# Performance work log

Measured on AMD Instinct MI355X. Metric: run time of the kernel, lower is better.

## Reference

```python
import jax, jax.numpy as jnp
import numpy as np

NUM_HEADS = 8
SCALE = 1.0
BN_EPS = 1e-5


def _mlp1d(x, W1, g1, b1, W2):
    # Conv1d(k=1, bias=False) -> BatchNorm1d (training-mode batch stats) -> ReLU -> Conv1d(k=1, bias=False)
    h = jnp.einsum('oi,bil->bol', W1, x)
    mu = h.mean(axis=(0, 2), keepdims=True)
    var = h.var(axis=(0, 2), keepdims=True)  # biased var, as torch BN training
    h = (h - mu) * jax.lax.rsqrt(var + BN_EPS)
    h = jax.nn.relu(h * g1[None, :, None] + b1[None, :, None])
    return jnp.einsum('oi,bil->bol', W2, h)


def setup_inputs() -> dict:
    key = jax.random.key(0)
    ks = jax.random.split(key, 8)
    b, c, hh, ww = 64, 2048, 14, 14
    hid, out = 4096, 256
    d = {'x': jax.random.normal(ks[0], (b, c, hh, ww), jnp.float32)}

    def w(k, o, i):
        return jax.random.normal(k, (o, i), jnp.float32) * np.float32(1.0 / np.sqrt(i))

    i = 1
    for pre in ('p', 'pp', 'po'):  # proj, proj_pixel, proj_obj
        d[pre + 'W1'] = w(ks[i], hid, c); i += 1
        d[pre + 'G1'] = jnp.ones((hid,), jnp.float32)
        d[pre + 'B1'] = jnp.zeros((hid,), jnp.float32)
        d[pre + 'W2'] = w(ks[i], out, hid); i += 1
    return d


def reference(x, pW1, pG1, pB1, pW2, ppW1, ppG1, ppB1, ppW2, poW1, poG1, poB1, poW2):
    b, c, h, w = x.shape
    xf = x.reshape(b, c, h * w)                      # flatten(2)
    x_pool = xf.mean(axis=2, keepdims=True)          # adaptive_avg_pool2d(x, 1)
    z_g = _mlp1d(x_pool, pW1, pG1, pB1, pW2)         # [b, 256, 1]
    z_feat = _mlp1d(xf, ppW1, ppG1, ppB1, ppW2)      # [b, 256, hw]
    # F.normalize(dim=1) with eps=1e-12, then /scale
    nrm = jnp.maximum(jnp.linalg.norm(z_feat, axis=1, keepdims=True), 1e-12)
    attn = (z_feat / nrm) / SCALE
    attn = attn.reshape(b, NUM_HEADS, -1, h * w)     # [b, nh, 256/nh, hw]
    attn = jax.nn.softmax(attn, axis=-1)
    x4 = xf.reshape(b, NUM_HEADS, c // NUM_HEADS, h * w)
    # torch.matmul(x, obj_attn.transpose(3, 2)) : [b,nh,c/nh,hw] @ [b,nh,hw,q]
    obj_val = jnp.einsum('bnkl,bnql->bnkq', x4, attn).reshape(b, c, -1)  # [b, c, 256/nh]
    obj_val = _mlp1d(obj_val, poW1, poG1, poB1, poW2)                    # [b, 256, 32]
    return z_g, obj_val
```

## Files before the change

### kernel.cpp

```cpp
#include <hip/hip_runtime.h>
#include <hip/hip_bf16.h>

using bf16 = __hip_bfloat16;
typedef __bf16 bf16x8v __attribute__((ext_vector_type(8)));
typedef float f32x4 __attribute__((ext_vector_type(4)));

#define BN_EPS 1e-5f

__device__ __forceinline__ void stval(float* p, float v) { *p = v; }
__device__ __forceinline__ void stval(bf16* p, float v)  { *p = __float2bfloat16(v); }

__device__ __forceinline__ void gload_lds16(const void* g, void* l) {
    __builtin_amdgcn_global_load_lds(
        (const __attribute__((address_space(1))) unsigned int*)g,
        (__attribute__((address_space(3))) unsigned int*)l,
        16, 0, 0);
}

__device__ __forceinline__ int xcd_swz(int orig, int nwg) {
    int q = nwg >> 3, r = nwg & 7;
    int xcd = orig & 7, idx = orig >> 3;
    return (xcd < r ? xcd * (q + 1) : r * (q + 1) + (xcd - r) * q) + idx;
}

template<typename TC>
__global__ __launch_bounds__(512, 2) void mfma_tn8(
    const bf16* __restrict__ A, const bf16* __restrict__ B, TC* __restrict__ C,
    int M, int N, int K, float* __restrict__ ps, float* __restrict__ pq)
{
    __shared__ char lds[131072];
    const int NT = K >> 6;
    const int tid = threadIdx.x;
    const int lane = tid & 63;
    const int wv = tid >> 6;
    const int wm = wv >> 2;
    const int wn = wv & 3;

    const int nbx = gridDim.x;
    int flat = blockIdx.y * nbx + blockIdx.x;
    const int cpx = (nbx * gridDim.y) >> 3;
    flat = (flat & 7) * cpx + (flat >> 3);
    const int mtile = flat / nbx;
    const long m0 = (long)mtile * 256;
    const long n0 = (long)(flat % nbx) * 256;

    const int trow = tid >> 3;
    const int ks = (((tid & 7) ^ ((tid >> 3) & 7)) << 3);
    const bf16* Arow0 = A + (m0 + trow) * (long)K + ks;
    const bf16* Brow0 = B + (n0 + trow) * (long)K + ks;
    char* ldsA = (char*)lds + tid * 16;
    char* ldsB = (char*)lds + 32768 + tid * 16;

    auto stage_a = [&](int bbuf, int kt) {
        const bf16* g = Arow0 + ((long)kt << 6);
        char* d = ldsA + (bbuf << 16);
        gload_lds16(g, d);
        gload_lds16(g + ((long)K << 6),  d + 8192);
        gload_lds16(g + ((long)K << 7),  d + 16384);
        gload_lds16(g + 192L * (long)K,  d + 24576);
    };
    auto stage_b = [&](int bbuf, int kt) {
        const bf16* g = Brow0 + ((long)kt << 6);
        char* d = ldsB + (bbuf << 16);
        gload_lds16(g, d);
        gload_lds16(g + ((long)K << 6),  d + 8192);
        gload_lds16(g + ((long)K << 7),  d + 16384);
        gload_lds16(g + 192L * (long)K,  d + 24576);
    };

    const int fr = lane & 15, fc = lane >> 4;
    const int ca0 = ((fc ^ (fr & 7)) << 4);
    const int ca1 = (((4 + fc) ^ (fr & 7)) << 4);

    f32x4 acc[8][4];
#pragma unroll
    for (int m = 0; m < 8; ++m)
#pragma unroll
        for (int n = 0; n < 4; ++n) acc[m][n] = (f32x4){0.f, 0.f, 0.f, 0.f};

    stage_a(0, 0); stage_b(0, 0); stage_a(1, 1); stage_b(1, 1);

    for (int T = 0; T < NT; ++T) {
        const int bb = T & 1;
        const char* Ard = (const char*)lds + (bb << 16) + (wm * 128 + fr) * 128;
        const char* Brd = (const char*)lds + (bb << 16) + 32768 + (wn * 64 + fr) * 128;

        if (T == 0)          { asm volatile("s_waitcnt vmcnt(8)" ::: "memory"); }
        else if (T < NT - 1) { asm volatile("s_waitcnt vmcnt(4)" ::: "memory"); }
        else                 { asm volatile("s_waitcnt vmcnt(0)" ::: "memory"); }
        __builtin_amdgcn_s_barrier();
        __builtin_amdgcn_sched_barrier(0);

        bf16x8v a0[8], a1[8];
#pragma unroll
        for (int m = 0; m < 8; ++m) {
            a0[m] = *(const bf16x8v*)(Ard + m * 2048 + ca0);
            a1[m] = *(const bf16x8v*)(Ard + m * 2048 + ca1);
        }
        bf16x8v b00 = *(const bf16x8v*)(Brd + ca0);
        bf16x8v b01 = *(const bf16x8v*)(Brd + ca1);
        bf16x8v b10 = *(const bf16x8v*)(Brd + 2048 + ca0);
        bf16x8v b11 = *(const bf16x8v*)(Brd + 2048 + ca1);

        if (T >= 1 && T + 1 < NT) stage_b(bb ^ 1, T + 1);

        __builtin_amdgcn_s_setprio(1);
#pragma unroll
        for (int m = 0; m < 8; ++m) {
            acc[m][0] = __builtin_amdgcn_mfma_f32_16x16x32_bf16(a0[m], b00, acc[m][0], 0, 0, 0);
            acc[m][0] = __builtin_amdgcn_mfma_f32_16x16x32_bf16(a1[m], b01, acc[m][0], 0, 0, 0);
            acc[m][1] = __builtin_amdgcn_mfma_f32_16x16x32_bf16(a0[m], b10, acc[m][1], 0, 0, 0);
            acc[m][1] = __builtin_amdgcn_mfma_f32_16x16x32_bf16(a1[m], b11, acc[m][1], 0, 0, 0);
        }
        __builtin_amdgcn_s_setprio(0);

        __builtin_amdgcn_s_barrier();
        __builtin_amdgcn_sched_barrier(0);

        bf16x8v b20 = *(const bf16x8v*)(Brd + 2 * 2048 + ca0);
        bf16x8v b21 = *(const bf16x8v*)(Brd + 2 * 2048 + ca1);
        bf16x8v b30 = *(const bf16x8v*)(Brd + 3 * 2048 + ca0);
        bf16x8v b31 = *(const bf16x8v*)(Brd + 3 * 2048 + ca1);

        if (T + 2 < NT) stage_a(bb, T + 2);

        __builtin_amdgcn_s_setprio(1);
#pragma unroll
        for (int m = 0; m < 8; ++m) {
            acc[m][2] = __builtin_amdgcn_mfma_f32_16x16x32_bf16(a0[m], b20, acc[m][2], 0, 0, 0);
            acc[m][2] = __builtin_amdgcn_mfma_f32_16x16x32_bf16(a1[m], b21, acc[m][2], 0, 0, 0);
            acc[m][3] = __builtin_amdgcn_mfma_f32_16x16x32_bf16(a0[m], b30, acc[m][3], 0, 0, 0);
            acc[m][3] = __builtin_amdgcn_mfma_f32_16x16x32_bf16(a1[m], b31, acc[m][3], 0, 0, 0);
        }
        __builtin_amdgcn_s_setprio(0);
    }

#pragma unroll
    for (int m = 0; m < 8; ++m) {
        long gr = m0 + wm * 128 + m * 16 + fc * 4;
#pragma unroll
        for (int n = 0; n < 4; ++n) {
            long gc = n0 + wn * 64 + n * 16 + fr;
            TC* cp = C + gr * N + gc;
#pragma unroll
            for (int r = 0; r < 4; ++r) stval(cp + (long)r * N, acc[m][n][r]);
        }
    }

    if (ps != nullptr) {
        __syncthreads();
        float* red = (float*)lds;
        float cs[4], cq[4];
#pragma unroll
        for (int n = 0; n < 4; ++n) {
            float s = 0.f, q = 0.f;
#pragma unroll
            for (int m = 0; m < 8; ++m)
#pragma unroll
                for (int r = 0; r < 4; ++r) {
                    float v = __bfloat162float(__float2bfloat16(acc[m][n][r]));
                    s += v; q += v * v;
                }
            s += __shfl_xor(s, 16, 64); s += __shfl_xor(s, 32, 64);
            q += __shfl_xor(q, 16, 64); q += __shfl_xor(q, 32, 64);
            cs[n] = s; cq[n] = q;
        }
        if (fc == 0) {
#pragma unroll
            for (int n = 0; n < 4; ++n) {
                red[wv * 64 + n * 16 + fr] = cs[n];
                red[512 + wv * 64 + n * 16 + fr] = cq[n];
            }
        }
        __syncthreads();
        if (tid < 256) {
            int c = tid, wnn = c >> 6, idx = c & 63;
            float s = red[wnn * 64 + idx] + red[(4 + wnn) * 64 + idx];
            float q = red[512 + wnn * 64 + idx] + red[512 + (4 + wnn) * 64 + idx];
            ps[(long)mtile * N + n0 + c] = s;
            pq[(long)mtile * N + n0 + c] = q;
        }
    }
}

template<typename TC>
__global__ __launch_bounds__(256) void mfma_tn(
    const bf16* __restrict__ A, const bf16* __restrict__ B, TC* __restrict__ C,
    int M, int N, int K, float* __restrict__ ps, float* __restrict__ pq)
{
    __shared__ alignas(16) unsigned short As[128 * 32];
    __shared__ alignas(16) unsigned short Bs[128 * 32];

    const int tid = threadIdx.x;
    const int l = tid & 63;
    const int nwg = gridDim.x * gridDim.y;
    int s = xcd_swz(blockIdx.y * gridDim.x + blockIdx.x, nwg);
    const int by = s / gridDim.x, bx = s % gridDim.x;
    const long m0 = (long)by * 128;
    const long n0 = (long)bx * 128;
    const int wr = (tid >> 7) & 1;
    const int wc = (tid >> 6) & 1;

    const int off0 = tid * 16;
    const int row0 = off0 >> 6;
    const int kp0  = (off0 >> 4) & 3;
    const bf16* Ag0 = A + (m0 + row0) * (long)K + kp0 * 8;
    const bf16* Ag1 = A + (m0 + row0 + 64) * (long)K + kp0 * 8;
    const bf16* Bg0 = B + (n0 + row0) * (long)K + kp0 * 8;
    const bf16* Bg1 = B + (n0 + row0 + 64) * (long)K + kp0 * 8;
    char* Asl0 = (char*)As + off0;
    char* Asl1 = (char*)As + off0 + 4096;
    char* Bsl0 = (char*)Bs + off0;
    char* Bsl1 = (char*)Bs + off0 + 4096;

    f32x4 acc[4][4];
#pragma unroll
    for (int m = 0; m < 4; ++m)
#pragma unroll
        for (int n = 0; n < 4; ++n) acc[m][n] = (f32x4){0.f, 0.f, 0.f, 0.f};

    const int fr = l & 15;
    const int fc = l >> 4;
    int aoff[4], boff[4];
#pragma unroll
    for (int m = 0; m < 4; ++m) aoff[m] = ((wr * 64 + m * 16 + fr) * 4 + fc) * 16;
#pragma unroll
    for (int n = 0; n < 4; ++n) boff[n] = ((wc * 64 + n * 16 + fr) * 4 + fc) * 16;

    for (int k0 = 0; k0 < K; k0 += 32) {
        gload_lds16(Ag0 + k0, Asl0);
        gload_lds16(Ag1 + k0, Asl1);
        gload_lds16(Bg0 + k0, Bsl0);
        gload_lds16(Bg1 + k0, Bsl1);
        __syncthreads();

        bf16x8v af[4], bfr[4];
#pragma unroll
        for (int m = 0; m < 4; ++m) af[m]  = *(const bf16x8v*)((const char*)As + aoff[m]);
#pragma unroll
        for (int n = 0; n < 4; ++n) bfr[n] = *(const bf16x8v*)((const char*)Bs + boff[n]);
#pragma unroll
        for (int m = 0; m < 4; ++m)
#pragma unroll
            for (int n = 0; n < 4; ++n)
                acc[m][n] = __builtin_amdgcn_mfma_f32_16x16x32_bf16(af[m], bfr[n], acc[m][n], 0, 0, 0);
        __syncthreads();
    }

#pragma unroll
    for (int m = 0; m < 4; ++m) {
        long gr = m0 + wr * 64 + m * 16 + fc * 4;
#pragma unroll
        for (int n = 0; n < 4; ++n) {
            long gc = n0 + wc * 64 + n * 16 + fr;
            TC* cp = C + gr * N + gc;
#pragma unroll
            for (int r = 0; r < 4; ++r) stval(cp + (long)r * N, acc[m][n][r]);
        }
    }

    if (ps != nullptr) {
        float* red = (float*)As;
        float cs[4], cq[4];
#pragma unroll
        for (int n = 0; n < 4; ++n) {
            float s2 = 0.f, q2 = 0.f;
#pragma unroll
            for (int m = 0; m < 4; ++m)
#pragma unroll
                for (int r = 0; r < 4; ++r) {
                    float v = __bfloat162float(__float2bfloat16(acc[m][n][r]));
                    s2 += v; q2 += v * v;
                }
            s2 += __shfl_xor(s2, 16, 64); s2 += __shfl_xor(s2, 32, 64);
            q2 += __shfl_xor(q2, 16, 64); q2 += __shfl_xor(q2, 32, 64);
            cs[n] = s2; cq[n] = q2;
        }
        if (fc == 0) {
#pragma unroll
            for (int n = 0; n < 4; ++n) {
                int c = wc * 64 + n * 16 + fr;
                red[wr * 128 + c] = cs[n];
                red[256 + wr * 128 + c] = cq[n];
            }
        }
        __syncthreads();
        if (tid < 128) {
            float sv = red[tid] + red[128 + tid];
            float qv = red[256 + tid] + red[384 + tid];
            ps[(long)by * N + n0 + tid] = sv;
            pq[(long)by * N + n0 + tid] = qv;
        }
    }
}

__global__ __launch_bounds__(256) void mfma_tn_skbn(
    const bf16* __restrict__ A, const bf16* __restrict__ B, float* __restrict__ Cp,
    int M, int N, int K, int KCH, const float* __restrict__ ta, const float* __restrict__ tc)
{
    __shared__ alignas(16) unsigned short As[128 * 32];
    __shared__ alignas(16) unsigned short Bs[128 * 32];

    const int tid = threadIdx.x;
    const int l = tid & 63;
    const int gxy = gridDim.x * gridDim.y;
    const int nwg = gxy * gridDim.z;
    int s = xcd_swz((blockIdx.z * gridDim.y + blockIdx.y) * gridDim.x + blockIdx.x, nwg);
    const int bz = s / gxy;
    const int rem = s % gxy;
    const int by = rem / gridDim.x, bx = rem % gridDim.x;
    const long m0 = (long)by * 128;
    const long n0 = (long)bx * 128;
    const int wr = (tid >> 7) & 1;
    const int wc = (tid >> 6) & 1;
    const int ksrt = bz * KCH;

    const int off0 = tid * 16;
    const int row0 = off0 >> 6;
    const int kp0  = (off0 >> 4) & 3;
    const bf16* Ag0 = A + (m0 + row0) * (long)K + kp0 * 8 + ksrt;
    const bf16* Ag1 = A + (m0 + row0 + 64) * (long)K + kp0 * 8 + ksrt;
    const bf16* Bg0 = B + (n0 + row0) * (long)K + kp0 * 8 + ksrt;
    const bf16* Bg1 = B + (n0 + row0 + 64) * (long)K + kp0 * 8 + ksrt;
    char* Asl0 = (char*)As + off0;
    char* Asl1 = (char*)As + off0 + 4096;
    char* Bsl0 = (char*)Bs + off0;
    char* Bsl1 = (char*)Bs + off0 + 4096;

    f32x4 acc[4][4];
#pragma unroll
    for (int m = 0; m < 4; ++m)
#pragma unroll
        for (int n = 0; n < 4; ++n) acc[m][n] = (f32x4){0.f, 0.f, 0.f, 0.f};

    const int fr = l & 15;
    const int fc = l >> 4;
    int aoff[4], boff[4];
#pragma unroll
    for (int m = 0; m < 4; ++m) aoff[m] = ((wr * 64 + m * 16 + fr) * 4 + fc) * 16;
#pragma unroll
    for (int n = 0; n < 4; ++n) boff[n] = ((wc * 64 + n * 16 + fr) * 4 + fc) * 16;

    for (int k0 = 0; k0 < KCH; k0 += 32) {
        gload_lds16(Bg0 + k0, Bsl0);
        gload_lds16(Bg1 + k0, Bsl1);

        union { bf16 h[8]; uint4 u; } r0, r1;
        r0.u = *(const uint4*)(Ag0 + k0);
        r1.u = *(const uint4*)(Ag1 + k0);
        const int kb = ksrt + k0 + kp0 * 8;
        float4 av0 = *(const float4*)(ta + kb);
        float4 av1 = *(const float4*)(ta + kb + 4);
        float4 cv0 = *(const float4*)(tc + kb);
        float4 cv1 = *(const float4*)(tc + kb + 4);
        float av[8] = {av0.x, av0.y, av0.z, av0.w, av1.x, av1.y, av1.z, av1.w};
        float cv[8] = {cv0.x, cv0.y, cv0.z, cv0.w, cv1.x, cv1.y, cv1.z, cv1.w};
#pragma unroll
        for (int j = 0; j < 8; ++j) {
            float v = fmaxf(fmaf(av[j], __bfloat162float(r0.h[j]), cv[j]), 0.f);
            r0.h[j] = __float2bfloat16(v);
            v = fmaxf(fmaf(av[j], __bfloat162float(r1.h[j]), cv[j]), 0.f);
            r1.h[j] = __float2bfloat16(v);
        }
        *(uint4*)Asl0 = r0.u;
        *(uint4*)Asl1 = r1.u;
        __syncthreads();

        bf16x8v af[4], bfr[4];
#pragma unroll
        for (int m = 0; m < 4; ++m) af[m]  = *(const bf16x8v*)((const char*)As + aoff[m]);
#pragma unroll
        for (int n = 0; n < 4; ++n) bfr[n] = *(const bf16x8v*)((const char*)Bs + boff[n]);
#pragma unroll
        for (int m = 0; m < 4; ++m)
#pragma unroll
            for (int n = 0; n < 4; ++n)
                acc[m][n] = __builtin_amdgcn_mfma_f32_16x16x32_bf16(af[m], bfr[n], acc[m][n], 0, 0, 0);
        __syncthreads();
    }

    float* Cb = Cp + (long)bz * M * N;
#pragma unroll
    for (int m = 0; m < 4; ++m) {
        long gr = m0 + wr * 64 + m * 16 + fc * 4;
#pragma unroll
        for (int n = 0; n < 4; ++n) {
            long gc = n0 + wc * 64 + n * 16 + fr;
            float* cp = Cb + gr * N + gc;
#pragma unroll
            for (int r = 0; r < 4; ++r) cp[(long)r * N] = acc[m][n][r];
        }
    }
}

__global__ __launch_bounds__(256) void objmm_k(
    const bf16* __restrict__ attnP, const bf16* __restrict__ xP, bf16* __restrict__ objinT)
{
    __shared__ alignas(16) unsigned short As[32 * 32];
    __shared__ alignas(16) unsigned short Bs[256 * 32];
    const int tid = threadIdx.x, lane = tid & 63, wv = tid >> 6;
    const int b = blockIdx.x >> 3, h = blockIdx.x & 7;
    const bf16* Ab = attnP + ((long)(b * 256 + h * 32)) * 224;
    const bf16* Bb = xP + ((long)(b * 2048 + h * 256)) * 224;
    const int fr = lane & 15, fc = lane >> 4;
    const int srow = tid >> 2, schk = tid & 3;

    f32x4 acc[2][4];
#pragma unroll
    for (int m = 0; m < 2; ++m)
#pragma unroll
        for (int n = 0; n < 4; ++n) acc[m][n] = (f32x4){0.f, 0.f, 0.f, 0.f};

    for (int k0 = 0; k0 < 224; k0 += 32) {
        if (wv < 2)
            gload_lds16(Ab + (long)srow * 224 + schk * 8 + k0, (char*)As + tid * 16);
#pragma unroll
        for (int j = 0; j < 4; ++j)
            gload_lds16(Bb + (long)(j * 64 + srow) * 224 + schk * 8 + k0,
                        (char*)Bs + j * 4096 + tid * 16);
        __syncthreads();

        bf16x8v af[2], bfr[4];
#pragma unroll
        for (int m = 0; m < 2; ++m)
            af[m] = *(const bf16x8v*)((const char*)As + (m * 16 + fr) * 64 + fc * 16);
#pragma unroll
        for (int n = 0; n < 4; ++n)
            bfr[n] = *(const bf16x8v*)((const char*)Bs + (wv * 64 + n * 16 + fr) * 64 + fc * 16);
#pragma unroll
        for (int m = 0; m < 2; ++m)
#pragma unroll
            for (int n = 0; n < 4; ++n)
                acc[m][n] = __builtin_amdgcn_mfma_f32_16x16x32_bf16(af[m], bfr[n], acc[m][n], 0, 0, 0);
        __syncthreads();
    }

#pragma unroll
    for (int m = 0; m < 2; ++m) {
        long gr = (long)b * 32 + m * 16 + fc * 4;
#pragma unroll
        for (int n = 0; n < 4; ++n) {
            long gc = (long)h * 256 + wv * 64 + n * 16 + fr;
            bf16* cp = objinT + gr * 2048 + gc;
#pragma unroll
            for (int r = 0; r < 4; ++r) cp[(long)r * 2048] = __float2bfloat16(acc[m][n][r]);
        }
    }
}

__global__ __launch_bounds__(256) void foldnorm_k(const float* __restrict__ p,
    float* __restrict__ z, float* __restrict__ invn)
{
    int j = blockIdx.x * 4 + (threadIdx.x >> 6);
    int lane = threadIdx.x & 63;
    long off = (long)j * 256 + lane * 4;
    float4 a = *(const float4*)(p + off);
    float4 b = *(const float4*)(p + 3211264L + off);
    float4 c = *(const float4*)(p + 2 * 3211264L + off);
    float4 d = *(const float4*)(p + 3 * 3211264L + off);
    float4 s;
    s.x = (a.x + b.x) + (c.x + d.x);
    s.y = (a.y + b.y) + (c.y + d.y);
    s.z = (a.z + b.z) + (c.z + d.z);
    s.w = (a.w + b.w) + (c.w + d.w);
    *(float4*)(z + off) = s;
    float q = s.x * s.x + s.y * s.y + s.z * s.z + s.w * s.w;
#pragma unroll
    for (int off2 = 32; off2; off2 >>= 1) q += __shfl_xor(q, off2, 64);
    if (lane == 0) invn[j] = 1.f / fmaxf(sqrtf(q), 1e-12f);
}

__global__ __launch_bounds__(256) void foldout_k(const float* __restrict__ p, float* __restrict__ out)
{
    int o = blockIdx.x * 256 + threadIdx.x;
    int b = o >> 13, rem = o & 8191, q = rem >> 5, tt = rem & 31;
    long base = ((long)(b * 32 + tt)) * 256 + q;
    float s = 0.f;
#pragma unroll
    for (int z = 0; z < 8; ++z) s += p[(long)z * 524288 + base];
    out[o] = s;
}

__global__ __launch_bounds__(256) void prep_k(
    const float* __restrict__ w1, const float* __restrict__ w2,
    const float* __restrict__ w3, const float* __restrict__ w4,
    bf16* __restrict__ o1, bf16* __restrict__ o2,
    bf16* __restrict__ o3, bf16* __restrict__ o4,
    const float* __restrict__ x, bf16* __restrict__ XT,
    bf16* __restrict__ xP, float* __restrict__ xpT)
{
    __shared__ unsigned short tile[196 * 66 + 4];
    __shared__ float pp[64];
    const int t = threadIdx.x;

    if (blockIdx.x < 9216) {
        const long L1 = 8388608, L2 = 1048576;
        long i = ((long)blockIdx.x * 256 + t) * 8;
        const float* src; bf16* dst; long e;
        if (i < L1)             { src = w1; dst = o1; e = i; }
        else if (i < L1 + L2)   { src = w2; dst = o2; e = i - L1; }
        else if (i < 2*L1 + L2) { src = w3; dst = o3; e = i - L1 - L2; }
        else                    { src = w4; dst = o4; e = i - 2*L1 - L2; }
        float4 v0 = *(const float4*)(src + e);
        float4 v1 = *(const float4*)(src + e + 4);
        union { bf16 h[8]; uint4 u; } r;
        r.h[0] = __float2bfloat16(v0.x); r.h[1] = __float2bfloat16(v0.y);
        r.h[2] = __float2bfloat16(v0.z); r.h[3] = __float2bfloat16(v0.w);
        r.h[4] = __float2bfloat16(v1.x); r.h[5] = __float2bfloat16(v1.y);
        r.h[6] = __float2bfloat16(v1.z); r.h[7] = __float2bfloat16(v1.w);
        *(uint4*)(dst + e) = r.u;
        return;
    }

    const int bid = blockIdx.x - 9216;
    const int b = bid >> 5, c0 = (bid & 31) * 64;
    const int wvi = t >> 6, lane = t & 63;

    for (int p = 0; p < 16; ++p) {
        int c = p * 4 + wvi;
        const float* row = x + ((long)b * 2048 + c0 + c) * 196;
        float v0 = row[lane];
        float v1 = row[lane + 64];
        float v2 = row[lane + 128];
        float v3 = (lane < 4) ? row[lane + 192] : 0.f;
        bf16 h0 = __float2bfloat16(v0);
        bf16 h1 = __float2bfloat16(v1);
        bf16 h2 = __float2bfloat16(v2);
        bf16 h3 = __float2bfloat16(v3);
        tile[lane * 66 + c]         = *(unsigned short*)&h0;
        tile[(lane + 64) * 66 + c]  = *(unsigned short*)&h1;
        tile[(lane + 128) * 66 + c] = *(unsigned short*)&h2;
        if (lane < 4) tile[(lane + 192) * 66 + c] = *(unsigned short*)&h3;
        float s = v0 + v1 + v2 + v3;
#pragma unroll
        for (int off = 32; off; off >>= 1) s += __shfl_xor(s, off, 64);
        if (lane == 0) pp[c] = s;
    }
    __syncthreads();
    if (t < 64) xpT[(c0 + t) * 64 + b] = pp[t] * (1.f / 196.f);

    for (int u = t; u < 196 * 8; u += 256) {
        int l = u >> 3, cc = u & 7;
        const unsigned short* sp = &tile[l * 66 + cc * 8];
        uint4 r;
        r.x = *(const unsigned int*)(sp);
        r.y = *(const unsigned int*)(sp + 2);
        r.z = *(const unsigned int*)(sp + 4);
        r.w = *(const unsigned int*)(sp + 6);
        *(uint4*)(&XT[((long)b * 196 + l) * 2048 + c0 + cc * 8]) = r;
    }

    for (int u = t; u < 64 * 28; u += 256) {
        int c = u / 28, ch = u % 28;
        int l0 = ch * 8;
        union { unsigned short h[8]; uint4 v; } r;
#pragma unroll
        for (int e = 0; e < 8; ++e) {
            int ll = l0 + e;
            r.h[e] = (ll < 196) ? tile[ll * 66 + c] : (unsigned short)0;
        }
        *(uint4*)(xP + ((long)b * 2048 + c0 + c) * 224 + l0) = r.v;
    }
}

__global__ __launch_bounds__(256) void colstat2_k(const float* __restrict__ ps, const float* __restrict__ pq,
    int P, float invN, const float* __restrict__ g, const float* __restrict__ be,
    float* __restrict__ ta, float* __restrict__ tc)
{
    int c = blockIdx.x * 256 + threadIdx.x;
    float s = 0.f, q = 0.f;
    for (int p = 0; p < P; ++p) { s += ps[(long)p * 4096 + c]; q += pq[(long)p * 4096 + c]; }
    float mu  = s * invN;
    float var = q * invN - mu * mu;
    float a   = g[c] * rsqrtf(var + BN_EPS);
    ta[c] = a;
    tc[c] = be[c] - mu * a;
}

__global__ __launch_bounds__(256) void softmax2_k(const float* __restrict__ z,
    const float* __restrict__ invn, bf16* __restrict__ attnP)
{
    int row  = blockIdx.x * 4 + (threadIdx.x >> 6);
    int lane = threadIdx.x & 63;
    int b = row >> 8, q = row & 255;
    float v[4];
    float mx = -INFINITY;
#pragma unroll
    for (int i = 0; i < 4; ++i) {
        int l = lane + 64 * i;
        if (l < 196) {
            int j = b * 196 + l;
            v[i] = z[(long)j * 256 + q] * invn[j];
        } else v[i] = -INFINITY;
        mx = fmaxf(mx, v[i]);
    }
#pragma unroll
    for (int off = 32; off; off >>= 1) mx = fmaxf(mx, __shfl_xor(mx, off, 64));
    float s = 0.f;
#pragma unroll
    for (int i = 0; i < 4; ++i) {
        v[i] = (lane + 64 * i < 196) ? __expf(v[i] - mx) : 0.f;
        s += v[i];
    }
#pragma unroll
    for (int off = 32; off; off >>= 1) s += __shfl_xor(s, off, 64);
    float is = 1.f / s;
    bf16* rp = attnP + (long)row * 224;
#pragma unroll
    for (int i = 0; i < 4; ++i) {
        int l = lane + 64 * i;
        if (l < 196) rp[l] = __float2bfloat16(v[i] * is);
        else if (l < 224) rp[l] = __float2bfloat16(0.f);
    }
}

template<bool TRANS>
__global__ __launch_bounds__(256) void gemmsk_k(
    const float* __restrict__ A, const float* __restrict__ B, float* __restrict__ Cp,
    int M, int N, int K, int lda, int ldbk, int KCH,
    const float* __restrict__ tra, const float* __restrict__ trc)
{
    constexpr int BM = 64, BN = 64, BK = 16;
    __shared__ float As[BK][BM + 4];
    __shared__ float Bs[BK][BN + 4];

    const int tid = threadIdx.x;
    const int m0 = blockIdx.y * BM;
    const int ks = blockIdx.z * KCH;
    const int ke = min(K, ks + KCH);

    const int tIdm = tid / 16;
    const int tIdn = tid % 16;
    const int aK  = tid % BK;
    const int aM0 = tid / BK;
    const int bN  = tid % BN;
    const int bK0 = tid / BN;

    float acc[4][4];
#pragma unroll
    for (int u = 0; u < 4; ++u)
#pragma unroll
        for (int v = 0; v < 4; ++v) acc[u][v] = 0.f;

    for (int k0 = ks; k0 < ke; k0 += BK) {
#pragma unroll
        for (int i = 0; i < 4; ++i) {
            int m = aM0 + 16 * i;
            int gk = k0 + aK, gm = m0 + m;
            float v = 0.f;
            if (gk < ke && gm < M) v = A[(long)gm * lda + gk];
            As[aK][m] = v;
        }
#pragma unroll
        for (int i = 0; i < 4; ++i) {
            int kk = bK0 + 4 * i;
            int gk = k0 + kk;
            float v = 0.f;
            if (gk < ke && bN < N) {
                v = B[(long)gk * ldbk + bN];
                if (TRANS) v = fmaxf(tra[gk] * v + trc[gk], 0.f);
            }
            Bs[kk][bN] = v;
        }
        __syncthreads();
#pragma unroll
        for (int kk = 0; kk < BK; ++kk) {
            float a[4], b[4];
#pragma unroll
            for (int u = 0; u < 4; ++u) a[u] = As[kk][tIdm * 4 + u];
#pragma unroll
            for (int v = 0; v < 4; ++v) b[v] = Bs[kk][tIdn * 4 + v];
#pragma unroll
            for (int u = 0; u < 4; ++u)
#pragma unroll
                for (int v = 0; v < 4; ++v)
                    acc[u][v] = fmaf(a[u], b[v], acc[u][v]);
        }
        __syncthreads();
    }

    float* Cb = Cp + (long)blockIdx.z * M * N;
#pragma unroll
    for (int u = 0; u < 4; ++u) {
        int gm = m0 + tIdm * 4 + u;
        if (gm >= M) continue;
#pragma unroll
        for (int v = 0; v < 4; ++v) {
            int gn = tIdn * 4 + v;
            if (gn < N) Cb[(long)gm * N + gn] = acc[u][v];
        }
    }
}

__global__ __launch_bounds__(256) void skbn_k(const float* __restrict__ Cp,
    const float* __restrict__ g, const float* __restrict__ be,
    float* __restrict__ h1, float* __restrict__ ta, float* __restrict__ tc)
{
    int o = blockIdx.x * 4 + (threadIdx.x >> 6);
    int b = threadIdx.x & 63;
    float s = 0.f;
#pragma unroll
    for (int p = 0; p < 16; ++p) s += Cp[(long)p * 262144 + o * 64 + b];
    h1[o * 64 + b] = s;
    float s1 = s, s2 = s * s;
#pragma unroll
    for (int off = 32; off; off >>= 1) {
        s1 += __shfl_down(s1, off, 64);
        s2 += __shfl_down(s2, off, 64);
    }
    if (b == 0) {
        float mu  = s1 * (1.f / 64.f);
        float var = s2 * (1.f / 64.f) - mu * mu;
        float a   = g[o] * rsqrtf(var + BN_EPS);
        ta[o] = a;
        tc[o] = be[o] - mu * a;
    }
}

__global__ __launch_bounds__(256) void skreduce_k(const float* __restrict__ Cp, int P, long MN,
    int Nn, int ldm, int ldn, float* __restrict__ out)
{
    long i = (long)blockIdx.x * 256 + threadIdx.x;
    if (i >= MN) return;
    float s = 0.f;
    for (int p = 0; p < P; ++p) s += Cp[(long)p * MN + i];
    int m = (int)(i / Nn), n = (int)(i % Nn);
    out[(long)m * ldm + (long)n * ldn] = s;
}

extern "C" void kernel_launch(void* const* d_in, const int* in_sizes, int n_in,
                              void* d_out, int out_size, void* d_ws, size_t ws_size,
                              hipStream_t stream)
{
    const float* x    = (const float*)d_in[0];
    const float* pW1  = (const float*)d_in[1];
    const float* pG1  = (const float*)d_in[2];
    const float* pB1  = (const float*)d_in[3];
    const float* pW2  = (const float*)d_in[4];
    const float* ppW1 = (const float*)d_in[5];
    const float* ppG1 = (const float*)d_in[6];
    const float* ppB1 = (const float*)d_in[7];
    const float* ppW2 = (const float*)d_in[8];
    const float* poW1 = (const float*)d_in[9];
    const float* poG1 = (const float*)d_in[10];
    const float* poB1 = (const float*)d_in[11];
    const float* poW2 = (const float*)d_in[12];
    float* out = (float*)d_out;
    (void)in_sizes; (void)n_in; (void)out_size; (void)ws_size;

    char* w = (char*)d_ws;
    auto alloc = [&](size_t bytes) -> char* {
        char* p = w; w += (bytes + 255) & ~(size_t)255; return p;
    };
    bf16* ppW1b = (bf16*)alloc((size_t)4096 * 2048 * 2);
    bf16* ppW2b = (bf16*)alloc((size_t)256 * 4096 * 2);
    bf16* poW1b = (bf16*)alloc((size_t)4096 * 2048 * 2);
    bf16* poW2b = (bf16*)alloc((size_t)256 * 4096 * 2);
    char* region1 = alloc((size_t)12544 * 2048 * 2);
    bf16*  XT     = (bf16*)region1;
    float* skpG2  = (float*)region1;
    bf16*  attnP  = (bf16*)region1;
    bf16*  objinT = (bf16*)(region1 + 12845056);
    bf16*  hobjT  = (bf16*)(region1 + 12845056 + 8388608);
    bf16* xP     = (bf16*)alloc((size_t)64 * 2048 * 224 * 2);
    bf16* hfeatT = (bf16*)alloc((size_t)12544 * 4096 * 2);
    float* zfeatT = (float*)alloc((size_t)12544 * 256 * 4);
    float* ps    = (float*)alloc((size_t)49 * 4096 * 4);
    float* pq    = (float*)alloc((size_t)49 * 4096 * 4);
    float* invn  = (float*)alloc((size_t)12544 * 4);
    float* a2    = (float*)alloc(4096 * 4);
    float* c2    = (float*)alloc(4096 * 4);
    float* a3    = (float*)alloc(4096 * 4);
    float* c3    = (float*)alloc(4096 * 4);
    float* xpT   = (float*)alloc((size_t)2048 * 64 * 4);
    float* h1    = (float*)alloc((size_t)4096 * 64 * 4);
    float* a1    = (float*)alloc(4096 * 4);
    float* c1    = (float*)alloc(4096 * 4);
    float* skp1  = (float*)alloc((size_t)16 * 4096 * 64 * 4);
    float* skp2  = (float*)alloc((size_t)32 * 256 * 64 * 4);
    float* skp5  = (float*)alloc((size_t)8 * 2048 * 256 * 4);

    prep_k<<<9216 + 2048, 256, 0, stream>>>(ppW1, ppW2, poW1, poW2,
                                            ppW1b, ppW2b, poW1b, poW2b,
                                            x, XT, xP, xpT);

    gemmsk_k<false><<<dim3(1, 64, 16), 256, 0, stream>>>(
        pW1, xpT, skp1, 4096, 64, 2048, 2048, 64, 128, nullptr, nullptr);
    skbn_k<<<1024, 256, 0, stream>>>(skp1, pG1, pB1, h1, a1, c1);
    gemmsk_k<true><<<dim3(1, 4, 32), 256, 0, stream>>>(
        pW2, h1, skp2, 256, 64, 4096, 4096, 64, 128, a1, c1);
    skreduce_k<<<64, 256, 0, stream>>>(skp2, 32, (long)256 * 64, 64, 1, 256, out);

    mfma_tn8<bf16><<<dim3(16, 49), 512, 0, stream>>>(XT, ppW1b, hfeatT, 12544, 4096, 2048, ps, pq);
    colstat2_k<<<16, 256, 0, stream>>>(ps, pq, 49, 1.f / 12544.f, ppG1, ppB1, a2, c2);

    mfma_tn_skbn<<<dim3(2, 98, 4), 256, 0, stream>>>(
        hfeatT, ppW2b, skpG2, 12544, 256, 4096, 1024, a2, c2);
    foldnorm_k<<<3136, 256, 0, stream>>>(skpG2, zfeatT, invn);

    softmax2_k<<<4096, 256, 0, stream>>>(zfeatT, invn, attnP);

    objmm_k<<<512, 256, 0, stream>>>(attnP, xP, objinT);

    mfma_tn<bf16><<<dim3(32, 16), 256, 0, stream>>>(objinT, poW1b, hobjT, 2048, 4096, 2048, ps, pq);
    colstat2_k<<<16, 256, 0, stream>>>(ps, pq, 16, 1.f / 2048.f, poG1, poB1, a3, c3);

    mfma_tn_skbn<<<dim3(2, 16, 8), 256, 0, stream>>>(
        hobjT, poW2b, skp5, 2048, 256, 4096, 512, a3, c3);
    foldout_k<<<2048, 256, 0, stream>>>(skp5, out + 16384);
}
```

Baseline: 609.7 us.

## Shrink big GEMM tile to 256x128 with K=32 steps and fold skreduce into foldnorm

Replaces the 256x256, K=64 tile of the main feature GEMM with a 256x128 tile using K=32 steps. It uses less LDS (48KB) and targets 4 blocks per CU, trading per-block reuse for higher occupancy and a larger grid. The LDS XOR swizzle is removed, so LDS bank conflicts may increase. The split-K reduction for z_g is also moved into extra blocks of foldnorm_k, removing one kernel launch.

Result: no change. 619.8 us (+1.7%).

```diff
diff --git a/kernel.cpp b/kernel.cpp
--- a/kernel.cpp
+++ b/kernel.cpp
@@ -23,18 +23,20 @@
     return (xcd < r ? xcd * (q + 1) : r * (q + 1) + (xcd - r) * q) + idx;
 }
 
+#define MFMA_BF16 __builtin_amdgcn_mfma_f32_16x16x32_bf16
+
 template<typename TC>
-__global__ __launch_bounds__(512, 2) void mfma_tn8(
+__global__ __launch_bounds__(512, 4) void mfma_tn8c(
     const bf16* __restrict__ A, const bf16* __restrict__ B, TC* __restrict__ C,
     int M, int N, int K, float* __restrict__ ps, float* __restrict__ pq)
 {
-    __shared__ char lds[131072];
-    const int NT = K >> 6;
+    __shared__ alignas(16) char lds[49152];
+    const int NT = K >> 5;
     const int tid = threadIdx.x;
     const int lane = tid & 63;
     const int wv = tid >> 6;
-    const int wm = wv >> 2;
-    const int wn = wv & 3;
+    const int wm = wv >> 1;
+    const int wn = wv & 1;
 
     const int nbx = gridDim.x;
     int flat = blockIdx.y * nbx + blockIdx.x;
@@ -42,39 +44,30 @@
     flat = (flat & 7) * cpx + (flat >> 3);
     const int mtile = flat / nbx;
     const long m0 = (long)mtile * 256;
-    const long n0 = (long)(flat % nbx) * 256;
-
-    const int trow = tid >> 3;
-    const int ks = (((tid & 7) ^ ((tid >> 3) & 7)) << 3);
-    const bf16* Arow0 = A + (m0 + trow) * (long)K + ks;
-    const bf16* Brow0 = B + (n0 + trow) * (long)K + ks;
-    char* ldsA = (char*)lds + tid * 16;
-    char* ldsB = (char*)lds + 32768 + tid * 16;
+    const long n0 = (long)(flat % nbx) * 128;
+
+    const int trow = tid >> 2;
+    const int tk   = (tid & 3) * 8;
+    const bf16* Ar = A + (m0 + trow) * (long)K + tk;
+    const bf16* Br = B + (n0 + trow) * (long)K + tk;
+    char* ldsAt = (char*)lds + tid * 16;
+    char* ldsBt = (char*)lds + 32768 + tid * 16;
 
     auto stage_a = [&](int bbuf, int kt) {
-        const bf16* g = Arow0 + ((long)kt << 6);
-        char* d = ldsA + (bbuf << 16);
+        const bf16* g = Ar + (kt << 5);
+        char* d = ldsAt + bbuf * 16384;
         gload_lds16(g, d);
-        gload_lds16(g + ((long)K << 6),  d + 8192);
-        gload_lds16(g + ((long)K << 7),  d + 16384);
-        gload_lds16(g + 192L * (long)K,  d + 24576);
+        gload_lds16(g + ((long)K << 7), d + 8192);
     };
     auto stage_b = [&](int bbuf, int kt) {
-        const bf16* g = Brow0 + ((long)kt << 6);
-        char* d = ldsB + (bbuf << 16);
-        gload_lds16(g, d);
-        gload_lds16(g + ((long)K << 6),  d + 8192);
-        gload_lds16(g + ((long)K << 7),  d + 16384);
-        gload_lds16(g + 192L * (long)K,  d + 24576);
+        gload_lds16(Br + (kt << 5), ldsBt + bbuf * 8192);
     };
 
     const int fr = lane & 15, fc = lane >> 4;
-    const int ca0 = ((fc ^ (fr & 7)) << 4);
-    const int ca1 = (((4 + fc) ^ (fr & 7)) << 4);
-
-    f32x4 acc[8][4];
-#pragma unroll
-    for (int m = 0; m < 8; ++m)
+
+    f32x4 acc[4][4];
+#pragma unroll
+    for (int m = 0; m < 4; ++m)
 #pragma unroll
         for (int n = 0; n < 4; ++n) acc[m][n] = (f32x4){0.f, 0.f, 0.f, 0.f};
 
@@ -82,62 +75,51 @@
 
     for (int T = 0; T < NT; ++T) {
         const int bb = T & 1;
-        const char* Ard = (const char*)lds + (bb << 16) + (wm * 128 + fr) * 128;
-        const char* Brd = (const char*)lds + (bb << 16) + 32768 + (wn * 64 + fr) * 128;
-
-        if (T == 0)          { asm volatile("s_waitcnt vmcnt(8)" ::: "memory"); }
-        else if (T < NT - 1) { asm volatile("s_waitcnt vmcnt(4)" ::: "memory"); }
+        const char* Ard = (const char*)lds + bb * 16384 + (wm * 64 + fr) * 64 + fc * 16;
+        const char* Brd = (const char*)lds + 32768 + bb * 8192 + (wn * 64 + fr) * 64 + fc * 16;
+
+        if (T == 0)          { asm volatile("s_waitcnt vmcnt(3)" ::: "memory"); }
+        else if (T < NT - 1) { asm volatile("s_waitcnt vmcnt(2)" ::: "memory"); }
         else                 { asm volatile("s_waitcnt vmcnt(0)" ::: "memory"); }
         __builtin_amdgcn_s_barrier();
         __builtin_amdgcn_sched_barrier(0);
 
-        bf16x8v a0[8], a1[8];
-#pragma unroll
-        for (int m = 0; m < 8; ++m) {
-            a0[m] = *(const bf16x8v*)(Ard + m * 2048 + ca0);
-            a1[m] = *(const bf16x8v*)(Ard + m * 2048 + ca1);
-        }
-        bf16x8v b00 = *(const bf16x8v*)(Brd + ca0);
-        bf16x8v b01 = *(const bf16x8v*)(Brd + ca1);
-        bf16x8v b10 = *(const bf16x8v*)(Brd + 2048 + ca0);
-        bf16x8v b11 = *(const bf16x8v*)(Brd + 2048 + ca1);
+        bf16x8v a[4];
+#pragma unroll
+        for (int m = 0; m < 4; ++m) a[m] = *(const bf16x8v*)(Ard + m * 1024);
+        bf16x8v b0 = *(const bf16x8v*)(Brd);
+        bf16x8v b1 = *(const bf16x8v*)(Brd + 1024);
 
         if (T >= 1 && T + 1 < NT) stage_b(bb ^ 1, T + 1);
 
         __builtin_amdgcn_s_setprio(1);
 #pragma unroll
-        for (int m = 0; m < 8; ++m) {
-            acc[m][0] = __builtin_amdgcn_mfma_f32_16x16x32_bf16(a0[m], b00, acc[m][0], 0, 0, 0);
-            acc[m][0] = __builtin_amdgcn_mfma_f32_16x16x32_bf16(a1[m], b01, acc[m][0], 0, 0, 0);
-            acc[m][1] = __builtin_amdgcn_mfma_f32_16x16x32_bf16(a0[m], b10, acc[m][1], 0, 0, 0);
-            acc[m][1] = __builtin_amdgcn_mfma_f32_16x16x32_bf16(a1[m], b11, acc[m][1], 0, 0, 0);
+        for (int m = 0; m < 4; ++m) {
+            acc[m][0] = MFMA_BF16(a[m], b0, acc[m][0], 0, 0, 0);
+            acc[m][1] = MFMA_BF16(a[m], b1, acc[m][1], 0, 0, 0);
         }
         __builtin_amdgcn_s_setprio(0);
 
         __builtin_amdgcn_s_barrier();
         __builtin_amdgcn_sched_barrier(0);
 
-        bf16x8v b20 = *(const bf16x8v*)(Brd + 2 * 2048 + ca0);
-        bf16x8v b21 = *(const bf16x8v*)(Brd + 2 * 2048 + ca1);
-        bf16x8v b30 = *(const bf16x8v*)(Brd + 3 * 2048 + ca0);
-        bf16x8v b31 = *(const bf16x8v*)(Brd + 3 * 2048 + ca1);
+        bf16x8v b2 = *(const bf16x8v*)(Brd + 2048);
+        bf16x8v b3 = *(const bf16x8v*)(Brd + 3072);
 
         if (T + 2 < NT) stage_a(bb, T + 2);
 
         __builtin_amdgcn_s_setprio(1);
 #pragma unroll
-        for (int m = 0; m < 8; ++m) {
-            acc[m][2] = __builtin_amdgcn_mfma_f32_16x16x32_bf16(a0[m], b20, acc[m][2], 0, 0, 0);
-            acc[m][2] = __builtin_amdgcn_mfma_f32_16x16x32_bf16(a1[m], b21, acc[m][2], 0, 0, 0);
-            acc[m][3] = __builtin_amdgcn_mfma_f32_16x16x32_bf16(a0[m], b30, acc[m][3], 0, 0, 0);
-            acc[m][3] = __builtin_amdgcn_mfma_f32_16x16x32_bf16(a1[m], b31, acc[m][3], 0, 0, 0);
+        for (int m = 0; m < 4; ++m) {
+            acc[m][2] = MFMA_BF16(a[m], b2, acc[m][2], 0, 0, 0);
+            acc[m][3] = MFMA_BF16(a[m], b3, acc[m][3], 0, 0, 0);
         }
         __builtin_amdgcn_s_setprio(0);
     }
 
 #pragma unroll
-    for (int m = 0; m < 8; ++m) {
-        long gr = m0 + wm * 128 + m * 16 + fc * 4;
+    for (int m = 0; m < 4; ++m) {
+        long gr = m0 + wm * 64 + m * 16 + fc * 4;
 #pragma unroll
         for (int n = 0; n < 4; ++n) {
             long gc = n0 + wn * 64 + n * 16 + fr;
@@ -155,7 +137,7 @@
         for (int n = 0; n < 4; ++n) {
             float s = 0.f, q = 0.f;
 #pragma unroll
-            for (int m = 0; m < 8; ++m)
+            for (int m = 0; m < 4; ++m)
 #pragma unroll
                 for (int r = 0; r < 4; ++r) {
                     float v = __bfloat162float(__float2bfloat16(acc[m][n][r]));
@@ -168,17 +150,17 @@
         if (fc == 0) {
 #pragma unroll
             for (int n = 0; n < 4; ++n) {
-                red[wv * 64 + n * 16 + fr] = cs[n];
-                red[512 + wv * 64 + n * 16 + fr] = cq[n];
+                int c = wn * 64 + n * 16 + fr;
+                red[wm * 128 + c] = cs[n];
+                red[512 + wm * 128 + c] = cq[n];
             }
         }
         __syncthreads();
-        if (tid < 256) {
-            int c = tid, wnn = c >> 6, idx = c & 63;
-            float s = red[wnn * 64 + idx] + red[(4 + wnn) * 64 + idx];
-            float q = red[512 + wnn * 64 + idx] + red[512 + (4 + wnn) * 64 + idx];
-            ps[(long)mtile * N + n0 + c] = s;
-            pq[(long)mtile * N + n0 + c] = q;
+        if (tid < 128) {
+            float s = red[tid] + red[128 + tid] + red[256 + tid] + red[384 + tid];
+            float q = red[512 + tid] + red[640 + tid] + red[768 + tid] + red[896 + tid];
+            ps[(long)mtile * N + n0 + tid] = s;
+            pq[(long)mtile * N + n0 + tid] = q;
         }
     }
 }
@@ -243,7 +225,7 @@
         for (int m = 0; m < 4; ++m)
 #pragma unroll
             for (int n = 0; n < 4; ++n)
-                acc[m][n] = __builtin_amdgcn_mfma_f32_16x16x32_bf16(af[m], bfr[n], acc[m][n], 0, 0, 0);
+                acc[m][n] = MFMA_BF16(af[m], bfr[n], acc[m][n], 0, 0, 0);
         __syncthreads();
     }
 
@@ -375,7 +357,7 @@
         for (int m = 0; m < 4; ++m)
 #pragma unroll
             for (int n = 0; n < 4; ++n)
-                acc[m][n] = __builtin_amdgcn_mfma_f32_16x16x32_bf16(af[m], bfr[n], acc[m][n], 0, 0, 0);
+                acc[m][n] = MFMA_BF16(af[m], bfr[n], acc[m][n], 0, 0, 0);
         __syncthreads();
     }
 
@@ -431,7 +413,7 @@
         for (int m = 0; m < 2; ++m)
 #pragma unroll
             for (int n = 0; n < 4; ++n)
-                acc[m][n] = __builtin_amdgcn_mfma_f32_16x16x32_bf16(af[m], bfr[n], acc[m][n], 0, 0, 0);
+                acc[m][n] = MFMA_BF16(af[m], bfr[n], acc[m][n], 0, 0, 0);
         __syncthreads();
     }
 
@@ -449,8 +431,17 @@
 }
 
 __global__ __launch_bounds__(256) void foldnorm_k(const float* __restrict__ p,
-    float* __restrict__ z, float* __restrict__ invn)
-{
+    float* __restrict__ z, float* __restrict__ invn,
+    const float* __restrict__ skp2, float* __restrict__ out)
+{
+    if (blockIdx.x >= 3136) {
+        int i = (blockIdx.x - 3136) * 256 + threadIdx.x;
+        float s = 0.f;
+        for (int pz = 0; pz < 32; ++pz) s += skp2[(long)pz * 16384 + i];
+        int m = i >> 6, n = i & 63;
+        out[m + n * 256] = s;
+        return;
+    }
     int j = blockIdx.x * 4 + (threadIdx.x >> 6);
     int lane = threadIdx.x & 63;
     long off = (long)j * 256 + lane * 4;
@@ -715,17 +706,6 @@
         ta[o] = a;
         tc[o] = be[o] - mu * a;
     }
-}
-
-__global__ __launch_bounds__(256) void skreduce_k(const float* __restrict__ Cp, int P, long MN,
-    int Nn, int ldm, int ldn, float* __restrict__ out)
-{
-    long i = (long)blockIdx.x * 256 + threadIdx.x;
-    if (i >= MN) return;
-    float s = 0.f;
-    for (int p = 0; p < P; ++p) s += Cp[(long)p * MN + i];
-    int m = (int)(i / Nn), n = (int)(i % Nn);
-    out[(long)m * ldm + (long)n * ldn] = s;
 }
 
 extern "C" void kernel_launch(void* const* d_in, const int* in_sizes, int n_in,
@@ -789,14 +769,13 @@
     skbn_k<<<1024, 256, 0, stream>>>(skp1, pG1, pB1, h1, a1, c1);
     gemmsk_k<true><<<dim3(1, 4, 32), 256, 0, stream>>>(
         pW2, h1, skp2, 256, 64, 4096, 4096, 64, 128, a1, c1);
-    skreduce_k<<<64, 256, 0, stream>>>(skp2, 32, (long)256 * 64, 64, 1, 256, out);
-
-    mfma_tn8<bf16><<<dim3(16, 49), 512, 0, stream>>>(XT, ppW1b, hfeatT, 12544, 4096, 2048, ps, pq);
+
+    mfma_tn8c<bf16><<<dim3(32, 49), 512, 0, stream>>>(XT, ppW1b, hfeatT, 12544, 4096, 2048, ps, pq);
     colstat2_k<<<16, 256, 0, stream>>>(ps, pq, 49, 1.f / 12544.f, ppG1, ppB1, a2, c2);
 
     mfma_tn_skbn<<<dim3(2, 98, 4), 256, 0, stream>>>(
         hfeatT, ppW2b, skpG2, 12544, 256, 4096, 1024, a2, c2);
-    foldnorm_k<<<3136, 256, 0, stream>>>(skpG2, zfeatT, invn);
+    foldnorm_k<<<3136 + 64, 256, 0, stream>>>(skpG2, zfeatT, invn, skp2, out);
 
     softmax2_k<<<4096, 256, 0, stream>>>(zfeatT, invn, attnP);
 
```
